# Performance work log

Hardware: AMD Instinct MI355X
Metric: run time of the kernel (lower is better)

Reference implementation:

```python
import jax, jax.numpy as jnp
import numpy as np

DIM = 64
HEADS = 4
EPS_LN = 1e-6
EPS_NORM = 1e-12


def _dwconv(x, w):
    # depthwise 3x3, SAME padding; x: [B,C,H,W], w: [C,1,3,3]
    return jax.lax.conv_general_dilated(
        x, w, window_strides=(1, 1), padding='SAME',
        feature_group_count=x.shape[1],
        dimension_numbers=('NCHW', 'OIHW', 'NCHW'))


def setup_inputs() -> dict:
    key = jax.random.key(0)
    ks = jax.random.split(key, 10)
    s = 0.05
    inp = {
        'x': jax.random.normal(ks[0], (8, DIM, 256, 256), dtype=jnp.float32),
        'ln_w': jnp.ones((DIM,), jnp.float32),
        'ln_b': jnp.zeros((DIM,), jnp.float32),
        'w_q': jax.random.normal(ks[1], (DIM, DIM), jnp.float32) * s,
        'w_k': jax.random.normal(ks[2], (DIM, DIM), jnp.float32) * s,
        'w_v': jax.random.normal(ks[3], (DIM, DIM), jnp.float32) * s,
        'dw_q': jax.random.normal(ks[4], (DIM, 1, 3, 3), jnp.float32) * s,
        'dw_k': jax.random.normal(ks[5], (DIM, 1, 3, 3), jnp.float32) * s,
        'dw_v': jax.random.normal(ks[6], (DIM, 1, 3, 3), jnp.float32) * s,
        'w_proj': jax.random.normal(ks[7], (DIM, DIM, 3, 3), jnp.float32) * s,
        'w_comp': jax.random.normal(ks[8], (DIM // 4, DIM), jnp.float32) * s,
        'temperature': jnp.ones((HEADS, 1, 1), jnp.float32),
    }
    return inp


def reference(x, ln_w, ln_b, w_q, w_k, w_v, dw_q, dw_k, dw_v, w_proj, w_comp, temperature):
    b, c, h, w = x.shape
    heads = temperature.shape[0]
    hd = c // heads  # per-head channels

    # LayerNorm over channel dim (per spatial location), biased variance
    mu = jnp.mean(x, axis=1, keepdims=True)
    var = jnp.mean((x - mu) ** 2, axis=1, keepdims=True)
    xn = (x - mu) / jnp.sqrt(var + EPS_LN)
    xn = xn * ln_w[None, :, None, None] + ln_b[None, :, None, None]

    # 1x1 projections then depthwise 3x3
    q = _dwconv(jnp.einsum('oc,bchw->bohw', w_q, xn), dw_q)
    k = _dwconv(jnp.einsum('oc,bchw->bohw', w_k, xn), dw_k)
    v = _dwconv(jnp.einsum('oc,bchw->bohw', w_v, xn), dw_v)

    # [b, heads, hd, h*w]
    q = q.reshape(b, heads, hd, h * w)
    k = k.reshape(b, heads, hd, h * w)
    v = v.reshape(b, heads, hd, h * w)

    # L2 normalize along spatial axis (torch F.normalize: x / max(||x||, eps))
    q = q / jnp.maximum(jnp.linalg.norm(q, axis=-1, keepdims=True), EPS_NORM)
    k = k / jnp.maximum(jnp.linalg.norm(k, axis=-1, keepdims=True), EPS_NORM)

    # channel attention: [b, heads, hd, hd]
    attn = jnp.einsum('bhcn,bhdn->bhcd', q, k) * temperature[None]
    attn = jax.nn.softmax(attn, axis=-1)
    out = jnp.einsum('bhcd,bhdn->bhcn', attn, v).reshape(b, c, h, w)

    # 3x3 projection + residual (residual is the normalized x, per source)
    out = jax.lax.conv_general_dilated(
        out, w_proj, window_strides=(1, 1), padding='SAME',
        dimension_numbers=('NCHW', 'OIHW', 'NCHW')) + xn

    # 1x1 compress to dim//4
    return jnp.einsum('oc,bchw->bohw', w_comp, out)
```

## Files before the change

### kernel.cpp

```cpp
#include <hip/hip_runtime.h>
#include <hip/hip_bf16.h>
#include <stdint.h>

#define BB 8
#define CC 64
#define HH 256
#define WW 256
#define NPIX 65536
#define HEADS 4
#define HD 16
#define PRS 76

using bf16 = __hip_bfloat16;
typedef __attribute__((ext_vector_type(8))) short short8;
typedef __attribute__((ext_vector_type(4))) float f32x4;

__device__ __forceinline__ float bf2f(bf16 v) { return __bfloat162float(v); }
__device__ __forceinline__ bf16 f2bf(float v) { return __float2bfloat16(v); }
__device__ __forceinline__ short f2bfs(float f) { bf16 h = __float2bfloat16(f); return *reinterpret_cast<short*>(&h); }
__device__ __forceinline__ float bfs2f(short s) { return __uint_as_float(((uint32_t)(uint16_t)s) << 16); }
__device__ __forceinline__ uint32_t pk2(float a, float b) {
  return (uint32_t)(uint16_t)f2bfs(a) | ((uint32_t)(uint16_t)f2bfs(b) << 16);
}
__device__ __forceinline__ short8 zero8() { short8 z = {0, 0, 0, 0, 0, 0, 0, 0}; return z; }

__global__ void k_prep(const float* __restrict__ w_comp, const float* __restrict__ w_proj,
                       const float* __restrict__ w_q, const float* __restrict__ w_k,
                       const float* __restrict__ w_v,
                       short* __restrict__ wcpb, short* __restrict__ wqkvb,
                       short* __restrict__ wcb) {
  int idx = blockIdx.x * 256 + threadIdx.x;
  if (idx < 9 * 16 * 64) {
    int c = idx & 63;
    int o = (idx >> 6) & 15;
    int kk = idx >> 10;
    float acc = 0.f;
    for (int m = 0; m < 64; ++m)
      acc += w_comp[o * 64 + m] * w_proj[(m * 64 + c) * 9 + kk];
    wcpb[idx] = f2bfs(acc);
  }
  if (idx < 3 * 4096) {
    const float* Ws[3] = {w_q, w_k, w_v};
    wqkvb[idx] = f2bfs(Ws[idx >> 12][idx & 4095]);
  }
  if (idx < 1024) wcb[idx] = f2bfs(w_comp[idx]);
}

__global__ __launch_bounds__(256)
void k_ln(const float* __restrict__ x, const float* __restrict__ ln_w,
          const float* __restrict__ ln_b, short* __restrict__ xnb) {
  const int tid = threadIdx.x;
  const int b = blockIdx.x >> 8;
  const int n = ((blockIdx.x & 255) << 8) + tid;
  const float* xp = x + (size_t)b * CC * NPIX + n;
  float v[64];
  float s = 0.f, s2 = 0.f;
#pragma unroll
  for (int c = 0; c < 64; ++c) {
    float t0 = xp[(size_t)c * NPIX];
    v[c] = t0; s += t0; s2 += t0 * t0;
  }
  const float mu = s * (1.f / 64.f);
  const float r = rsqrtf(s2 * (1.f / 64.f) - mu * mu + 1e-6f);
  short* op = xnb + ((size_t)b * NPIX + n) * 64;
#pragma unroll
  for (int c8 = 0; c8 < 8; ++c8) {
    uint32_t pk[4];
#pragma unroll
    for (int j = 0; j < 4; ++j) {
      const int c0 = c8 * 8 + 2 * j;
      float f0 = (v[c0] - mu) * r * ln_w[c0] + ln_b[c0];
      float f1 = (v[c0 + 1] - mu) * r * ln_w[c0 + 1] + ln_b[c0 + 1];
      pk[j] = pk2(f0, f1);
    }
    *reinterpret_cast<uint4*>(op + c8 * 8) = make_uint4(pk[0], pk[1], pk[2], pk[3]);
  }
}

__global__ __launch_bounds__(512)
void k_qkv(const short* __restrict__ xnb, const short* __restrict__ wqkvb,
           const short* __restrict__ wcb,
           const float* __restrict__ dw_q, const float* __restrict__ dw_k,
           const float* __restrict__ dw_v,
           bf16* __restrict__ qo, bf16* __restrict__ ko,
           short* __restrict__ aov, short* __restrict__ res16) {
  __shared__ short pr_s[336 * PRS];
  const int tid = threadIdx.x;
  const int lane = tid & 63;
  const int wv = tid >> 6;
  const int olocal = lane & 15;
  const int g = lane >> 4;
  const int t = blockIdx.y;
  const int tx = blockIdx.x & 15, ty = (blockIdx.x >> 4) & 15, b = blockIdx.x >> 8;
  const int x0 = tx * 16 - 1, y0 = ty * 16 - 1;

  if (t == 0) {
    short8 wc0 = *reinterpret_cast<const short8*>(wcb + olocal * 64 + g * 8);
    short8 wc1 = *reinterpret_cast<const short8*>(wcb + olocal * 64 + 32 + g * 8);
#pragma unroll
    for (int t2 = 0; t2 < 2; ++t2) {
      const int oy = wv * 2 + t2;
      const int n = (ty * 16 + oy) * WW + tx * 16 + olocal;
      const short* bb = xnb + ((size_t)b * NPIX + n) * 64 + g * 8;
      short8 b0 = *reinterpret_cast<const short8*>(bb);
      short8 b1 = *reinterpret_cast<const short8*>(bb + 32);
      f32x4 acc = {0.f, 0.f, 0.f, 0.f};
      acc = __builtin_amdgcn_mfma_f32_16x16x32_bf16(wc0, b0, acc, 0, 0, 0);
      acc = __builtin_amdgcn_mfma_f32_16x16x32_bf16(wc1, b1, acc, 0, 0, 0);
      uint2 st;
      st.x = pk2(acc[0], acc[1]);
      st.y = pk2(acc[2], acc[3]);
      *reinterpret_cast<uint2*>(&res16[((size_t)b * NPIX + n) * 16 + g * 4]) = st;
    }
  }

  short8 Bt[4][2];
#pragma unroll
  for (int ot = 0; ot < 4; ++ot) {
    const short* wb = wqkvb + t * 4096 + (ot * 16 + olocal) * 64 + g * 8;
    Bt[ot][0] = *reinterpret_cast<const short8*>(wb);
    Bt[ot][1] = *reinterpret_cast<const short8*>(wb + 32);
  }

  short8 a0[3], a1[3];
#pragma unroll
  for (int j = 0; j < 3; ++j) {
    const int pt = wv + j * 8;
    const int p = pt * 16 + olocal;
    const int py = y0 + p / 18;
    const int px_ = x0 + p % 18;
    const bool vld = (pt < 21) && (p < 324) && ((unsigned)py < 256u) && ((unsigned)px_ < 256u);
    if (vld) {
      const short* ab = xnb + ((size_t)b * NPIX + py * WW + px_) * 64 + g * 8;
      a0[j] = *reinterpret_cast<const short8*>(ab);
      a1[j] = *reinterpret_cast<const short8*>(ab + 32);
    } else {
      a0[j] = zero8();
      a1[j] = zero8();
    }
  }
#pragma unroll
  for (int j = 0; j < 3; ++j) {
    const int pt = wv + j * 8;
    if (pt >= 21) continue;
    const int p2 = pt * 16 + olocal;
#pragma unroll
    for (int ot = 0; ot < 4; ++ot) {
      f32x4 acc = {0.f, 0.f, 0.f, 0.f};
      acc = __builtin_amdgcn_mfma_f32_16x16x32_bf16(Bt[ot][0], a0[j], acc, 0, 0, 0);
      acc = __builtin_amdgcn_mfma_f32_16x16x32_bf16(Bt[ot][1], a1[j], acc, 0, 0, 0);
      uint2 st;
      st.x = pk2(acc[0], acc[1]);
      st.y = pk2(acc[2], acc[3]);
      *reinterpret_cast<uint2*>(&pr_s[p2 * PRS + ot * 16 + g * 4]) = st;
    }
  }
  __syncthreads();

  const float* dmt = (t == 0) ? dw_q : (t == 1) ? dw_k : dw_v;
  float dmr[8][9];
#pragma unroll
  for (int u = 0; u < 8; ++u)
#pragma unroll
    for (int kk = 0; kk < 9; ++kk)
      dmr[u][kk] = dmt[(wv * 8 + u) * 9 + kk];
  bf16* ob = ((t == 0) ? qo : ko) + (size_t)b * CC * NPIX;
#pragma unroll
  for (int i = 0; i < 4; ++i) {
    const int pxl = lane + i * 64;
    const int oy = pxl >> 4, ox = pxl & 15;
    float acc8[8] = {0.f, 0.f, 0.f, 0.f, 0.f, 0.f, 0.f, 0.f};
#pragma unroll
    for (int ky = 0; ky < 3; ++ky)
#pragma unroll
      for (int kx = 0; kx < 3; ++kx) {
        const short8 pv = *reinterpret_cast<const short8*>(
            &pr_s[((oy + ky) * 18 + ox + kx) * PRS + wv * 8]);
        const int kk = ky * 3 + kx;
#pragma unroll
        for (int u = 0; u < 8; ++u)
          acc8[u] += dmr[u][kk] * bfs2f(pv[u]);
      }
    const int n = (ty * 16 + oy) * WW + tx * 16 + ox;
    if (t < 2) {
#pragma unroll
      for (int u = 0; u < 8; ++u)
        ob[(size_t)(wv * 8 + u) * NPIX + n] = f2bf(acc8[u]);
    } else {
      uint4 st = make_uint4(pk2(acc8[0], acc8[1]), pk2(acc8[2], acc8[3]),
                            pk2(acc8[4], acc8[5]), pk2(acc8[6], acc8[7]));
      *reinterpret_cast<uint4*>(&aov[((size_t)b * NPIX + n) * 64 + wv * 8]) = st;
    }
  }
}

__global__ __launch_bounds__(256)
void k_logits(const bf16* __restrict__ q, const bf16* __restrict__ kk_,
              float* __restrict__ Spart, float* __restrict__ Qpart,
              float* __restrict__ Kpart) {
  const int tid = threadIdx.x;
  const int lane = tid & 63;
  const int wv = tid >> 6;
  const int bh = blockIdx.x >> 6;
  const int chunk = blockIdx.x & 63;
  const int row = lane & 15;
  const int g = lane >> 4;
  const short* qp = (const short*)q + (size_t)(bh * HD + row) * NPIX;
  const short* kp = (const short*)kk_ + (size_t)(bh * HD + row) * NPIX;
  const int n0 = chunk * 1024 + wv * 256 + g * 8;
  f32x4 s = {0.f, 0.f, 0.f, 0.f};
  f32x4 sq = {0.f, 0.f, 0.f, 0.f};
  f32x4 sk = {0.f, 0.f, 0.f, 0.f};
#pragma unroll
  for (int it = 0; it < 8; ++it) {
    const int n = n0 + it * 32;
    short8 qa = *reinterpret_cast<const short8*>(qp + n);
    short8 ka = *reinterpret_cast<const short8*>(kp + n);
    s  = __builtin_amdgcn_mfma_f32_16x16x32_bf16(qa, ka, s, 0, 0, 0);
    sq = __builtin_amdgcn_mfma_f32_16x16x32_bf16(qa, qa, sq, 0, 0, 0);
    sk = __builtin_amdgcn_mfma_f32_16x16x32_bf16(ka, ka, sk, 0, 0, 0);
  }
  const size_t tile = (size_t)blockIdx.x * 4 + wv;
  float* sp = Spart + tile * 256;
#pragma unroll
  for (int r = 0; r < 4; ++r)
    sp[(g * 4 + r) * 16 + row] = s[r];
  if ((row >> 2) == g) {
    Qpart[tile * 16 + row] = sq[row & 3];
    Kpart[tile * 16 + row] = sk[row & 3];
  }
}

__global__ __launch_bounds__(256)
void k_softmax(const float* __restrict__ Spart, const float* __restrict__ Qpart,
               const float* __restrict__ Kpart, const float* __restrict__ temp,
               short* __restrict__ attb) {
  const int tid = threadIdx.x;
  const int bh = blockIdx.x;
  const int b = bh >> 2, h = bh & 3;
  const int i = tid >> 4, j = tid & 15;
  float S = 0.f, qs = 0.f, ks = 0.f;
  const size_t t0 = (size_t)bh * 256;
  for (int c = 0; c < 256; ++c) {
    S += Spart[(t0 + c) * 256 + tid];
    qs += Qpart[(t0 + c) * 16 + i];
    ks += Kpart[(t0 + c) * 16 + j];
  }
  float nq = fmaxf(sqrtf(qs), 1e-12f);
  float nk = fmaxf(sqrtf(ks), 1e-12f);
  float val = S / (nq * nk) * temp[h];
  float m = val;
  for (int d = 1; d < 16; d <<= 1) m = fmaxf(m, __shfl_xor(m, d));
  float e = __expf(val - m);
  float s = e;
  for (int d = 1; d < 16; d <<= 1) s += __shfl_xor(s, d);
  attb[((size_t)b * 64 + h * 16 + i) * 64 + h * 16 + j] = f2bfs(e / s);
#pragma unroll
  for (int mq = 0; mq < 4; ++mq) {
    const int idx = tid * 4 + mq;
    const int r = idx >> 6, c = idx & 63;
    if ((c >> 4) != h)
      attb[((size_t)b * 64 + h * 16 + r) * 64 + c] = 0;
  }
}

__global__ __launch_bounds__(512)
void k_attf(const short* __restrict__ attb, const short* __restrict__ vao,
            const short* __restrict__ wcpb, const short* __restrict__ res16,
            float* __restrict__ out) {
  __shared__ short ao_s[336 * PRS];
  const int tid = threadIdx.x;
  const int lane = tid & 63;
  const int wv = tid >> 6;
  const int olocal = lane & 15;
  const int g = lane >> 4;
  const int tx = blockIdx.x & 15, ty = (blockIdx.x >> 4) & 15, b = blockIdx.x >> 8;
  const int x0 = tx * 16 - 1, y0 = ty * 16 - 1;

  {
    short8 AT[4][2];
#pragma unroll
    for (int ot = 0; ot < 4; ++ot) {
      const short* ab = attb + ((size_t)b * 64 + ot * 16 + olocal) * 64 + g * 8;
      AT[ot][0] = *reinterpret_cast<const short8*>(ab);
      AT[ot][1] = *reinterpret_cast<const short8*>(ab + 32);
    }
#pragma unroll
    for (int j = 0; j < 3; ++j) {
      const int pt = wv + j * 8;
      if (pt >= 21) continue;
      const int p = pt * 16 + olocal;
      const int py = y0 + p / 18;
      const int px_ = x0 + p % 18;
      const bool vld = (p < 324) && ((unsigned)py < 256u) && ((unsigned)px_ < 256u);
      short8 b0 = zero8(), b1 = zero8();
      if (vld) {
        const short* vp = vao + ((size_t)b * NPIX + py * WW + px_) * 64 + g * 8;
        b0 = *reinterpret_cast<const short8*>(vp);
        b1 = *reinterpret_cast<const short8*>(vp + 32);
      }
#pragma unroll
      for (int ot = 0; ot < 4; ++ot) {
        f32x4 acc = {0.f, 0.f, 0.f, 0.f};
        acc = __builtin_amdgcn_mfma_f32_16x16x32_bf16(AT[ot][0], b0, acc, 0, 0, 0);
        acc = __builtin_amdgcn_mfma_f32_16x16x32_bf16(AT[ot][1], b1, acc, 0, 0, 0);
        uint2 st;
        st.x = pk2(acc[0], acc[1]);
        st.y = pk2(acc[2], acc[3]);
        *reinterpret_cast<uint2*>(&ao_s[p * PRS + ot * 16 + g * 4]) = st;
      }
    }
  }
  __syncthreads();

  short8 WA[9][2];
#pragma unroll
  for (int kk = 0; kk < 9; ++kk) {
    const short* wb = wcpb + (kk * 16 + olocal) * 64 + g * 8;
    WA[kk][0] = *reinterpret_cast<const short8*>(wb);
    WA[kk][1] = *reinterpret_cast<const short8*>(wb + 32);
  }
#pragma unroll
  for (int s = 0; s < 2; ++s) {
    const int oy = wv * 2 + s;
    const int n0 = (ty * 16 + oy) * WW + tx * 16;
    uint2 rv = *reinterpret_cast<const uint2*>(
        &res16[((size_t)b * NPIX + n0 + olocal) * 16 + g * 4]);
    f32x4 acc;
    acc[0] = __uint_as_float(rv.x << 16);
    acc[1] = __uint_as_float(rv.x & 0xffff0000u);
    acc[2] = __uint_as_float(rv.y << 16);
    acc[3] = __uint_as_float(rv.y & 0xffff0000u);
#pragma unroll
    for (int ky = 0; ky < 3; ++ky)
#pragma unroll
      for (int kx = 0; kx < 3; ++kx) {
        const int hp = (oy + ky) * 18 + olocal + kx;
        short8 b0 = *reinterpret_cast<const short8*>(&ao_s[hp * PRS + g * 8]);
        short8 b1 = *reinterpret_cast<const short8*>(&ao_s[hp * PRS + 32 + g * 8]);
        acc = __builtin_amdgcn_mfma_f32_16x16x32_bf16(WA[ky * 3 + kx][0], b0, acc, 0, 0, 0);
        acc = __builtin_amdgcn_mfma_f32_16x16x32_bf16(WA[ky * 3 + kx][1], b1, acc, 0, 0, 0);
      }
    float* op = out + ((size_t)b * 16 + g * 4) * NPIX + n0 + olocal;
    op[0] = acc[0];
    op[NPIX] = acc[1];
    op[2 * NPIX] = acc[2];
    op[3 * NPIX] = acc[3];
  }
}

extern "C" void kernel_launch(void* const* d_in, const int* in_sizes, int n_in,
                              void* d_out, int out_size, void* d_ws, size_t ws_size,
                              hipStream_t stream) {
  const float* x      = (const float*)d_in[0];
  const float* ln_w   = (const float*)d_in[1];
  const float* ln_b   = (const float*)d_in[2];
  const float* w_q    = (const float*)d_in[3];
  const float* w_k    = (const float*)d_in[4];
  const float* w_v    = (const float*)d_in[5];
  const float* dw_q   = (const float*)d_in[6];
  const float* dw_k   = (const float*)d_in[7];
  const float* dw_v   = (const float*)d_in[8];
  const float* w_proj = (const float*)d_in[9];
  const float* w_comp = (const float*)d_in[10];
  const float* temp   = (const float*)d_in[11];
  float* out = (float*)d_out;

  const size_t SPX = (size_t)BB * NPIX;
  short* xnb   = (short*)d_ws;
  short* qb    = xnb + SPX * 64;
  short* kb    = qb + SPX * 64;
  short* aov   = kb + SPX * 64;
  short* res16 = aov + SPX * 64;
  short* wcpb  = res16 + SPX * 16;
  short* wqkvb = wcpb + 9216;
  short* wcb   = wqkvb + 12288;
  short* attb  = wcb + 1024;
  float* Spart = (float*)(attb + 8 * 64 * 64 + 512);
  float* Qpart = Spart + 32 * 256 * 256;
  float* Kpart = Qpart + 32 * 256 * 16;

  k_prep<<<52, 256, 0, stream>>>(w_comp, w_proj, w_q, w_k, w_v, wcpb, wqkvb, wcb);
  k_ln<<<2048, 256, 0, stream>>>(x, ln_w, ln_b, xnb);
  dim3 gqkv(2048, 3);
  k_qkv<<<gqkv, 512, 0, stream>>>(xnb, wqkvb, wcb, dw_q, dw_k, dw_v,
                                  (bf16*)qb, (bf16*)kb, aov, res16);
  k_logits<<<2048, 256, 0, stream>>>((const bf16*)qb, (const bf16*)kb, Spart, Qpart, Kpart);
  k_softmax<<<32, 256, 0, stream>>>(Spart, Qpart, Kpart, temp, attb);
  k_attf<<<2048, 512, 0, stream>>>(attb, aov, wcpb, res16, out);
}
```

Baseline: 320.6 us.

## Compute depthwise 3x3 conv with MFMA using diagonal weight matrices

Replaces the scalar FMA depthwise 3x3 convolution in the QKV kernel with MFMA instructions. The prep kernel builds block-diagonal bf16 weight matrices per tap (zero-padded to ten taps), and each wave runs MFMAs over pixel rows read from the shared projection tile. This moves the depthwise arithmetic onto the matrix cores and removes per-thread weight loads into registers. In exchange it spends most MFMA work on zeros, changes the global store pattern (scalar strided stores for q/k, non-vector stores for v), and quantizes the depthwise weights to bf16.

```diff
diff --git a/kernel.cpp b/kernel.cpp
--- a/kernel.cpp
+++ b/kernel.cpp
@@ -27,8 +27,10 @@
 __global__ void k_prep(const float* __restrict__ w_comp, const float* __restrict__ w_proj,
                        const float* __restrict__ w_q, const float* __restrict__ w_k,
                        const float* __restrict__ w_v,
+                       const float* __restrict__ dw_q, const float* __restrict__ dw_k,
+                       const float* __restrict__ dw_v,
                        short* __restrict__ wcpb, short* __restrict__ wqkvb,
-                       short* __restrict__ wcb) {
+                       short* __restrict__ wcb, short* __restrict__ ddiag) {
   int idx = blockIdx.x * 256 + threadIdx.x;
   if (idx < 9 * 16 * 64) {
     int c = idx & 63;
@@ -44,6 +46,15 @@
     wqkvb[idx] = f2bfs(Ws[idx >> 12][idx & 4095]);
   }
   if (idx < 1024) wcb[idx] = f2bfs(w_comp[idx]);
+  if (idx < 3 * 64 * 160) {
+    const float* Ds[3] = {dw_q, dw_k, dw_v};
+    int t = idx / 10240;
+    int c = (idx / 160) % 64;
+    int k = idx % 160;
+    int tap = k >> 4, c16 = k & 15;
+    float v = (tap < 9 && c16 == (c & 15)) ? Ds[t][c * 9 + tap] : 0.f;
+    ddiag[idx] = f2bfs(v);
+  }
 }
 
 __global__ __launch_bounds__(256)
@@ -79,9 +90,7 @@
 
 __global__ __launch_bounds__(512)
 void k_qkv(const short* __restrict__ xnb, const short* __restrict__ wqkvb,
-           const short* __restrict__ wcb,
-           const float* __restrict__ dw_q, const float* __restrict__ dw_k,
-           const float* __restrict__ dw_v,
+           const short* __restrict__ wcb, const short* __restrict__ ddiag,
            bf16* __restrict__ qo, bf16* __restrict__ ko,
            short* __restrict__ aov, short* __restrict__ res16) {
   __shared__ short pr_s[336 * PRS];
@@ -155,41 +164,58 @@
       *reinterpret_cast<uint2*>(&pr_s[p2 * PRS + ot * 16 + g * 4]) = st;
     }
   }
+
+  short8 AD[4][5];
+#pragma unroll
+  for (int ot = 0; ot < 4; ++ot)
+#pragma unroll
+    for (int kc = 0; kc < 5; ++kc)
+      AD[ot][kc] = *reinterpret_cast<const short8*>(
+          ddiag + (t * 64 + ot * 16 + olocal) * 160 + kc * 32 + g * 8);
+
   __syncthreads();
 
-  const float* dmt = (t == 0) ? dw_q : (t == 1) ? dw_k : dw_v;
-  float dmr[8][9];
-#pragma unroll
-  for (int u = 0; u < 8; ++u)
-#pragma unroll
-    for (int kk = 0; kk < 9; ++kk)
-      dmr[u][kk] = dmt[(wv * 8 + u) * 9 + kk];
   bf16* ob = ((t == 0) ? qo : ko) + (size_t)b * CC * NPIX;
 #pragma unroll
-  for (int i = 0; i < 4; ++i) {
-    const int pxl = lane + i * 64;
-    const int oy = pxl >> 4, ox = pxl & 15;
-    float acc8[8] = {0.f, 0.f, 0.f, 0.f, 0.f, 0.f, 0.f, 0.f};
-#pragma unroll
-    for (int ky = 0; ky < 3; ++ky)
-#pragma unroll
-      for (int kx = 0; kx < 3; ++kx) {
-        const short8 pv = *reinterpret_cast<const short8*>(
-            &pr_s[((oy + ky) * 18 + ox + kx) * PRS + wv * 8]);
-        const int kk = ky * 3 + kx;
-#pragma unroll
-        for (int u = 0; u < 8; ++u)
-          acc8[u] += dmr[u][kk] * bfs2f(pv[u]);
+  for (int s = 0; s < 2; ++s) {
+    const int tt = wv * 2 + s;
+    f32x4 acc[4] = {{0.f,0.f,0.f,0.f},{0.f,0.f,0.f,0.f},{0.f,0.f,0.f,0.f},{0.f,0.f,0.f,0.f}};
+#pragma unroll
+    for (int kc = 0; kc < 5; ++kc) {
+      int tap = kc * 2 + (g >> 1);
+      if (tap > 8) tap = 8;
+      const int ky = tap / 3, kx = tap % 3;
+      const int row = (tt + ky) * 18 + olocal + kx;
+      if (t < 2) {
+#pragma unroll
+        for (int ot = 0; ot < 4; ++ot) {
+          short8 Bf = *reinterpret_cast<const short8*>(
+              &pr_s[row * PRS + ot * 16 + (g & 1) * 8]);
+          acc[ot] = __builtin_amdgcn_mfma_f32_16x16x32_bf16(AD[ot][kc], Bf, acc[ot], 0, 0, 0);
+        }
+      } else {
+#pragma unroll
+        for (int ot = 0; ot < 4; ++ot) {
+          short8 Bf = *reinterpret_cast<const short8*>(
+              &pr_s[row * PRS + ot * 16 + (g & 1) * 8]);
+          acc[ot] = __builtin_amdgcn_mfma_f32_16x16x32_bf16(Bf, AD[ot][kc], acc[ot], 0, 0, 0);
+        }
       }
-    const int n = (ty * 16 + oy) * WW + tx * 16 + ox;
+    }
+    const int rowbase = (ty * 16 + tt) * WW + tx * 16;
     if (t < 2) {
 #pragma unroll
-      for (int u = 0; u < 8; ++u)
-        ob[(size_t)(wv * 8 + u) * NPIX + n] = f2bf(acc8[u]);
+      for (int ot = 0; ot < 4; ++ot)
+#pragma unroll
+        for (int r = 0; r < 4; ++r)
+          ob[(size_t)(ot * 16 + g * 4 + r) * NPIX + rowbase + olocal] = f2bf(acc[ot][r]);
     } else {
-      uint4 st = make_uint4(pk2(acc8[0], acc8[1]), pk2(acc8[2], acc8[3]),
-                            pk2(acc8[4], acc8[5]), pk2(acc8[6], acc8[7]));
-      *reinterpret_cast<uint4*>(&aov[((size_t)b * NPIX + n) * 64 + wv * 8]) = st;
+#pragma unroll
+      for (int ot = 0; ot < 4; ++ot)
+#pragma unroll
+        for (int r = 0; r < 4; ++r)
+          aov[((size_t)b * NPIX + rowbase + g * 4 + r) * 64 + ot * 16 + olocal] =
+              f2bfs(acc[ot][r]);
     }
   }
 }
@@ -375,15 +401,17 @@
   short* wcpb  = res16 + SPX * 16;
   short* wqkvb = wcpb + 9216;
   short* wcb   = wqkvb + 12288;
-  short* attb  = wcb + 1024;
+  short* ddiag = wcb + 1024;
+  short* attb  = ddiag + 30720;
   float* Spart = (float*)(attb + 8 * 64 * 64 + 512);
   float* Qpart = Spart + 32 * 256 * 256;
   float* Kpart = Qpart + 32 * 256 * 16;
 
-  k_prep<<<52, 256, 0, stream>>>(w_comp, w_proj, w_q, w_k, w_v, wcpb, wqkvb, wcb);
+  k_prep<<<120, 256, 0, stream>>>(w_comp, w_proj, w_q, w_k, w_v,
+                                  dw_q, dw_k, dw_v, wcpb, wqkvb, wcb, ddiag);
   k_ln<<<2048, 256, 0, stream>>>(x, ln_w, ln_b, xnb);
   dim3 gqkv(2048, 3);
-  k_qkv<<<gqkv, 512, 0, stream>>>(xnb, wqkvb, wcb, dw_q, dw_k, dw_v,
+  k_qkv<<<gqkv, 512, 0, stream>>>(xnb, wqkvb, wcb, ddiag,
                                   (bf16*)qb, (bf16*)kb, aov, res16);
   k_logits<<<2048, 256, 0, stream>>>((const bf16*)qb, (const bf16*)kb, Spart, Qpart, Kpart);
   k_softmax<<<32, 256, 0, stream>>>(Spart, Qpart, Kpart, temp, attb);
```

Result: slower. 354.2 us (+10.5%).
